# Kernel optimization log

Measured on AMD Instinct MI355X. Metric: run time of the kernel, lower is better.

## Reference

```python
import jax, jax.numpy as jnp
import numpy as np

B = 32
SIZES = [5023, 1256, 314, 79]
NS = [s + 1 for s in SIZES]   # padded vertex counts per level: [5024,1257,315,80]
K = 9
ENC_C = [3, 64, 128, 256]
DEC_C = [256, 128, 64, 3]
LATENT = 256


def _feast(x, nbr, wm, bm, wc, bc, act):
    # x: [B,N,F]; nbr: [N,K] int32 (col 0 = self index)
    xn = jnp.transpose(x[:, nbr, :], (0, 1, 3, 2))          # [B,N,F,K]
    xr = xn - xn[..., :1]                                    # relative to self neighbor
    logits = jnp.einsum('bnfk,of->bnok', xr, wm) + bm[None, None, :, None]  # conv1d(F->K,1)
    perm = jax.nn.softmax(logits, axis=2)                    # softmax over out-channel dim (torch dim=1)
    agg = jnp.einsum('bnfk,bnko->bnfo', xn, perm)            # [B,N,F,K] batched matmul
    Bv, N, F, Kv = agg.shape
    y = act(agg.reshape(Bv, N, F * Kv) @ wc.T + bc)          # linear(F*K -> out)
    mask = jnp.ones((N, 1), y.dtype).at[-1, 0].set(0.0)      # zero out padding vertex
    return y * mask


def _pool(x, L):
    # x: [B,M,F]; L: [Mp,M] -> [B,Mp,F]  (dense form of torch.spmm pooling)
    return jnp.einsum('pm,bmf->bpf', L, x)


def _forward(x, nbrs, Ds, Us, enc_p, dec_p, fce_w, fce_b, fcd_w, fcd_b):
    elu = jax.nn.elu
    ident = lambda v: v
    for i in range(3):
        wm, bm, wc, bc = enc_p[i]
        x = _feast(x, nbrs[i], wm, bm, wc, bc, elu)
        x = _pool(x, Ds[i])
    z = x.reshape(B, -1) @ fce_w.T + fce_b                    # [B, latent]
    x = (z @ fcd_w.T + fcd_b).reshape(B, NS[3], DEC_C[0])
    dec_nbrs = [nbrs[2], nbrs[1], nbrs[0]]
    dec_Us = [Us[2], Us[1], Us[0]]
    acts = [elu, elu, ident]                                  # last dconv uses identity
    for i in range(3):
        x = _pool(x, dec_Us[i])
        wm, bm, wc, bc = dec_p[i]
        x = _feast(x, dec_nbrs[i], wm, bm, wc, bc, acts[i])
    return x


def setup_inputs() -> dict:
    key = jax.random.key(0)
    ks = iter(jax.random.split(key, 64))
    nrm = lambda sh, s=0.05: jax.random.normal(next(ks), sh, dtype=jnp.float32) * s
    inp = {}
    inp['x'] = jax.random.normal(next(ks), (B, NS[0], 3), dtype=jnp.float32)
    for i in range(3):
        n = NS[i]
        nb = jax.random.randint(next(ks), (n, K), 0, n)
        nb = nb.at[:, 0].set(jnp.arange(n))
        inp[f'nbr{i}'] = nb.astype(jnp.int32)
    for i in range(3):
        cols = jax.random.randint(next(ks), (NS[i + 1],), 0, NS[i])
        inp[f'D{i}'] = jax.nn.one_hot(cols, NS[i], dtype=jnp.float32)   # sparse-like pooling
        cols_u = jax.random.randint(next(ks), (NS[i],), 0, NS[i + 1])
        inp[f'U{i}'] = jax.nn.one_hot(cols_u, NS[i + 1], dtype=jnp.float32)
    for i in range(3):
        fi, fo = ENC_C[i], ENC_C[i + 1]
        inp[f'e{i}_wm'] = nrm((K, fi)); inp[f'e{i}_bm'] = jnp.zeros((K,), jnp.float32)
        inp[f'e{i}_wc'] = nrm((fo, fi * K)); inp[f'e{i}_bc'] = jnp.zeros((fo,), jnp.float32)
    inp['fce_w'] = nrm((LATENT, NS[3] * ENC_C[3])); inp['fce_b'] = jnp.zeros((LATENT,), jnp.float32)
    inp['fcd_w'] = nrm((NS[3] * DEC_C[0], LATENT)); inp['fcd_b'] = jnp.zeros((NS[3] * DEC_C[0],), jnp.float32)
    for i in range(3):
        fi, fo = DEC_C[i], DEC_C[i + 1]
        inp[f'd{i}_wm'] = nrm((K, fi)); inp[f'd{i}_bm'] = jnp.zeros((K,), jnp.float32)
        inp[f'd{i}_wc'] = nrm((fo, fi * K)); inp[f'd{i}_bc'] = jnp.zeros((fo,), jnp.float32)
    return inp


def reference(x, nbr0, nbr1, nbr2, D0, D1, D2, U0, U1, U2,
              e0_wm, e0_bm, e0_wc, e0_bc, e1_wm, e1_bm, e1_wc, e1_bc,
              e2_wm, e2_bm, e2_wc, e2_bc, fce_w, fce_b, fcd_w, fcd_b,
              d0_wm, d0_bm, d0_wc, d0_bc, d1_wm, d1_bm, d1_wc, d1_bc,
              d2_wm, d2_bm, d2_wc, d2_bc):
    nbrs = [nbr0, nbr1, nbr2]
    Ds = [D0, D1, D2]
    Us = [U0, U1, U2]
    enc_p = [(e0_wm, e0_bm, e0_wc, e0_bc), (e1_wm, e1_bm, e1_wc, e1_bc), (e2_wm, e2_bm, e2_wc, e2_bc)]
    dec_p = [(d0_wm, d0_bm, d0_wc, d0_bc), (d1_wm, d1_bm, d1_wc, d1_bc), (d2_wm, d2_bm, d2_wc, d2_bc)]
    return _forward(x, nbrs, Ds, Us, enc_p, dec_p, fce_w, fce_b, fcd_w, fcd_b)
```

## Files before the change

### kernel.cpp

```cpp
#include <hip/hip_runtime.h>
#include <cstddef>

#define KN 9
typedef unsigned short u16;
typedef unsigned int u32;
typedef __attribute__((ext_vector_type(8))) short short8;
typedef __attribute__((ext_vector_type(4))) float f32x4;

__device__ inline u16 f2b(float f) {
    union { float f; u32 u; } v; v.f = f;
    u32 r = v.u + 0x7FFFu + ((v.u >> 16) & 1u);
    return (u16)(r >> 16);
}
__device__ inline float b2f(u16 h) {
    union { u32 u; float f; } v; v.u = ((u32)h) << 16; return v.f;
}

__device__ inline int xcd_swz(int bid, int n) {
    int q = n >> 3, r = n & 7;
    int x = bid & 7, pos = bid >> 3;
    return (x < r ? x * (q + 1) : r * (q + 1) + (x - r) * q) + pos;
}

__global__ void extract_idx_all(
    const float* __restrict__ D0, const float* __restrict__ D1, const float* __restrict__ D2,
    const float* __restrict__ U0, const float* __restrict__ U1, const float* __restrict__ U2,
    int* __restrict__ iD0, int* __restrict__ iD1, int* __restrict__ iD2,
    int* __restrict__ iU0, int* __restrict__ iU1, int* __restrict__ iU2)
{
    int blk = blockIdx.x;
    const float* L; int M; int* out; int p;
    if      (blk < 1257) { L = D0; M = 5024; out = iD0; p = blk; }
    else if (blk < 1572) { L = D1; M = 1257; out = iD1; p = blk - 1257; }
    else if (blk < 1652) { L = D2; M = 315;  out = iD2; p = blk - 1572; }
    else if (blk < 6676) { L = U0; M = 1257; out = iU0; p = blk - 1652; }
    else if (blk < 7933) { L = U1; M = 315;  out = iU1; p = blk - 6676; }
    else                 { L = U2; M = 80;   out = iU2; p = blk - 7933; }
    const float* row = L + (size_t)p * M;
    for (int m = threadIdx.x; m < M; m += 256)
        if (row[m] > 0.5f) out[p] = m;
}

__global__ void zero_f32(float4* __restrict__ p, int n4)
{
    int t = blockIdx.x * 256 + threadIdx.x;
    if (t < n4) p[t] = (float4){0.f, 0.f, 0.f, 0.f};
}

__device__ inline void wcr_one(const float* __restrict__ wc, u16* __restrict__ out, int t, int F) {
    int FK = F * KN;
    int c = t / FK, rem = t - c * FK, j = rem / F, f = rem - j * F;
    out[t] = f2b(wc[(size_t)c * FK + f * KN + j]);
}
__device__ inline void wg_one(const float* __restrict__ wc, u16* __restrict__ out, int t, int F, int C) {
    int n = t / F, f = t - n * F;
    int j = n / C, c = n - j * C;
    out[t] = f2b(wc[(size_t)c * (F * KN) + f * KN + j]);
}
__device__ inline void ccw_one(const float* __restrict__ wm, u16* __restrict__ out, int t, int F) {
    int n = t / F, f = t - n * F;
    out[t] = (n < KN) ? f2b(wm[n * F + f]) : (u16)0;
}
__global__ void cvt_weights(
    const float* __restrict__ e1_wc, const float* __restrict__ e2_wc,
    const float* __restrict__ d0_wc, const float* __restrict__ d1_wc,
    const float* __restrict__ e1_wm, const float* __restrict__ e2_wm,
    const float* __restrict__ d0_wm, const float* __restrict__ d1_wm,
    const float* __restrict__ d2_wm, const float* __restrict__ d2_wc,
    u16* __restrict__ wcrE1, u16* __restrict__ wcrE2,
    u16* __restrict__ wg0, u16* __restrict__ wg1,
    u16* __restrict__ ccwE1, u16* __restrict__ ccwE2,
    u16* __restrict__ ccwD0, u16* __restrict__ ccwD1,
    u16* __restrict__ w3, float* __restrict__ zbuf)
{
    int t = blockIdx.x * 256 + threadIdx.x;
    if (t < 73728)  { wcr_one(e1_wc, wcrE1, t, 64);       return; } t -= 73728;
    if (t < 294912) { wcr_one(e2_wc, wcrE2, t, 128);      return; } t -= 294912;
    if (t < 294912) { wg_one(d0_wc, wg0, t, 256, 128);    return; } t -= 294912;
    if (t < 73728)  { wg_one(d1_wc, wg1, t, 128, 64);     return; } t -= 73728;
    if (t < 4096)   { ccw_one(e1_wm, ccwE1, t, 64);       return; } t -= 4096;
    if (t < 8192)   { ccw_one(e2_wm, ccwE2, t, 128);      return; } t -= 8192;
    if (t < 16384)  { ccw_one(d0_wm, ccwD0, t, 256);      return; } t -= 16384;
    if (t < 8192)   { ccw_one(d1_wm, ccwD1, t, 128);      return; } t -= 8192;
    if (t < 4096) {
        int n = t >> 6, k = t & 63;
        float v = 0.f;
        if (n < KN) v = d2_wm[n * 64 + k];
        else if (n >= 9 && n < 36) {
            int cj = n - 9, j = cj / 3, c = cj - j * 3;
            v = d2_wc[(size_t)c * 576 + k * KN + j];
        }
        w3[t] = f2b(v);
        return;
    } t -= 4096;
    if (t < 8192) zbuf[t] = 0.f;
}

__global__ void compose_tables(
    const int* __restrict__ nbr0, const int* __restrict__ nbr1, const int* __restrict__ nbr2,
    const int* __restrict__ idxD1, const int* __restrict__ idxD2,
    const int* __restrict__ idxU0, const int* __restrict__ idxU1, const int* __restrict__ idxU2,
    int* __restrict__ nbrD1, int* __restrict__ nbrD2,
    int* __restrict__ nbrU2, int* __restrict__ nbrU1, int* __restrict__ nbrU0,
    int* __restrict__ maskE1, int* __restrict__ maskE2)
{
    int t = blockIdx.x * 256 + threadIdx.x;
    if (t < 2835)  { int p = t / 9, j = t - p * 9; nbrD1[p * 12 + j] = nbr1[idxD1[p] * 9 + j]; return; } t -= 2835;
    if (t < 720)   { int p = t / 9, j = t - p * 9; nbrD2[p * 12 + j] = nbr2[idxD2[p] * 9 + j]; return; } t -= 720;
    if (t < 2835)  { int p = t / 9, j = t - p * 9; nbrU2[p * 12 + j] = idxU2[nbr2[p * 9 + j]]; return; } t -= 2835;
    if (t < 11313) { int p = t / 9, j = t - p * 9; nbrU1[p * 12 + j] = idxU1[nbr1[p * 9 + j]]; return; } t -= 11313;
    if (t < 45216) { int p = t / 9, j = t - p * 9; nbrU0[p * 12 + j] = idxU0[nbr0[p * 9 + j]]; return; } t -= 45216;
    if (t < 315)   { maskE1[t] = (idxD1[t] == 1256) ? 1 : 0; return; } t -= 315;
    if (t < 80)    { maskE2[t] = (idxD2[t] == 314) ? 1 : 0; }
}

template<int NW, int OS>
__global__ __launch_bounds__(256) void cc_gemm(
    const u16* __restrict__ A, const u16* __restrict__ W,
    float* __restrict__ out, int M, int F)
{
    __shared__ u16 As[64 * 72];
    __shared__ u16 Ws[64 * 72];
    int tid = threadIdx.x;
    int mT = blockIdx.x * 64;
    int wid = tid >> 6, lane = tid & 63;
    int wr = wid >> 1, wcq = wid & 1;
    int r = lane & 15, g = lane >> 4;
    f32x4 acc[2][2];
    #pragma unroll
    for (int i = 0; i < 2; ++i)
        #pragma unroll
        for (int j = 0; j < 2; ++j)
            acc[i][j] = (f32x4){0.f, 0.f, 0.f, 0.f};

    for (int k0 = 0; k0 < F; k0 += 64) {
        #pragma unroll
// ... 49 lines not shown
    int wr = wid >> 1, wcq = wid & 1;
    int r = lane & 15, g = lane >> 4;
    f32x4 acc[2][2];
    #pragma unroll
    for (int i = 0; i < 2; ++i)
        #pragma unroll
        for (int j = 0; j < 2; ++j)
            acc[i][j] = (f32x4){0.f, 0.f, 0.f, 0.f};

    {
        #pragma unroll
        for (int h = 0; h < 2; ++h) {
            int gi = tid + h * 256;
            int m = gi >> 3, kg = gi & 7;
            uint4 va = {0u, 0u, 0u, 0u};
            int row = mT + m;
            if (row < M) va = *(const uint4*)(A + (size_t)row * 64 + kg * 8);
            *(uint4*)&As[m * 72 + kg * 8] = va;
            *(uint4*)&Ws[m * 72 + kg * 8] = *(const uint4*)(W + (size_t)m * 64 + kg * 8);
        }
        __syncthreads();
        #pragma unroll
        for (int S = 0; S < 2; ++S) {
            short8 af[2], bf[2];
            #pragma unroll
            for (int R = 0; R < 2; ++R)
                af[R] = *(const short8*)&As[(wr * 32 + R * 16 + r) * 72 + S * 32 + g * 8];
            #pragma unroll
            for (int C2 = 0; C2 < 2; ++C2)
                bf[C2] = *(const short8*)&Ws[(wcq * 32 + C2 * 16 + r) * 72 + S * 32 + g * 8];
            #pragma unroll
            for (int R = 0; R < 2; ++R)
                #pragma unroll
                for (int C2 = 0; C2 < 2; ++C2)
                    acc[R][C2] = __builtin_amdgcn_mfma_f32_16x16x32_bf16(af[R], bf[C2], acc[R][C2], 0, 0, 0);
        }
    }
    #pragma unroll
    for (int R = 0; R < 2; ++R)
        #pragma unroll
        for (int C2 = 0; C2 < 2; ++C2)
            #pragma unroll
            for (int q = 0; q < 4; ++q) {
                int mm = mT + wr * 32 + R * 16 + g * 4 + q;
                if (mm >= M) continue;
                int nn = wcq * 32 + C2 * 16 + r;
                if (nn >= 36) continue;
                int b = mm / 1257, p = mm - b * 1257;
                float val = acc[R][C2][q];
                if (nn < 9) {
                    CCT[((size_t)p * 9 + nn) * 32 + b] = val;
                } else {
                    int cj = nn - 9, j = cj / 3, c = cj - j * 3;
                    GWT[(size_t)p * 864 + j * 96 + b * 3 + c] = val;
                }
            }
}

template<int ACT, int MASK>
__global__ __launch_bounds__(256) void lin_gemm(
    const u16* __restrict__ A, const u16* __restrict__ W,
    const float* __restrict__ bias, u16* __restrict__ Y,
    const int* __restrict__ maskT,
    int M, int K, int N, int P)
{
    __shared__ u16 As[2][64 * 72];
    __shared__ u16 Ws[2][64 * 72];
    int tid = threadIdx.x;
    int mT = blockIdx.x * 64, nT = blockIdx.y * 64;
    int wid = tid >> 6, lane = tid & 63;
    int wr = wid >> 1, wcq = wid & 1;
    int r = lane & 15, g = lane >> 4;
    int lm = tid >> 3, lkg = tid & 7;
    f32x4 acc[2][2];
    #pragma unroll
    for (int i = 0; i < 2; ++i)
        #pragma unroll
        for (int j = 0; j < 2; ++j)
            acc[i][j] = (f32x4){0.f, 0.f, 0.f, 0.f};

    uint4 ra[2], rw[2];
    #pragma unroll
    for (int h = 0; h < 2; ++h) {
        int m = lm + h * 32;
        int row = mT + m;
        uint4 z; z.x = z.y = z.z = z.w = 0u;
        ra[h] = (row < M) ? *(const uint4*)(A + (size_t)row * K + lkg * 8) : z;
        rw[h] = *(const uint4*)(W + (size_t)(nT + m) * K + lkg * 8);
    }
    #pragma unroll
    for (int h = 0; h < 2; ++h) {
        int m = lm + h * 32;
        *(uint4*)&As[0][m * 72 + lkg * 8] = ra[h];
        *(uint4*)&Ws[0][m * 72 + lkg * 8] = rw[h];
    }

    int cur = 0;
    for (int k0 = 0; k0 < K; k0 += 64) {
        __syncthreads();
        bool more = (k0 + 64 < K);
        if (more) {
            int kn = k0 + 64;
            #pragma unroll
            for (int h = 0; h < 2; ++h) {
                int m = lm + h * 32;
                int row = mT + m;
                uint4 z; z.x = z.y = z.z = z.w = 0u;
// ... 56 lines not shown
    int wid = tid >> 6, lane = tid & 63;
    int wr = wid >> 1, wcq = wid & 1;
    int r = lane & 15, g = lane >> 4;
    f32x4 acc[2][2];
    #pragma unroll
    for (int i = 0; i < 2; ++i)
        #pragma unroll
        for (int j = 0; j < 2; ++j)
            acc[i][j] = (f32x4){0.f, 0.f, 0.f, 0.f};

    for (int s = 0; s < KSTEPS; ++s) {
        int k0 = kbase + s * 64;
        #pragma unroll
        for (int h = 0; h < 2; ++h) {
            int gi = tid + h * 256;
            int m = gi >> 3, kg = gi & 7;
            uint4 va = {0u, 0u, 0u, 0u};
            int row = mT + m;
            if (row < M) va = *(const uint4*)(A + (size_t)row * K + k0 + kg * 8);
            *(uint4*)&As[m * 72 + kg * 8] = va;
            *(uint4*)&Ws[m * 72 + kg * 8] = *(const uint4*)(W + (size_t)(nT + m) * K + k0 + kg * 8);
        }
        __syncthreads();
        #pragma unroll
        for (int S = 0; S < 2; ++S) {
            short8 af[2], bf[2];
            #pragma unroll
            for (int R = 0; R < 2; ++R)
                af[R] = *(const short8*)&As[(wr * 32 + R * 16 + r) * 72 + S * 32 + g * 8];
            #pragma unroll
            for (int C2 = 0; C2 < 2; ++C2)
                bf[C2] = *(const short8*)&Ws[(wcq * 32 + C2 * 16 + r) * 72 + S * 32 + g * 8];
            #pragma unroll
            for (int R = 0; R < 2; ++R)
                #pragma unroll
                for (int C2 = 0; C2 < 2; ++C2)
                    acc[R][C2] = __builtin_amdgcn_mfma_f32_16x16x32_bf16(af[R], bf[C2], acc[R][C2], 0, 0, 0);
        }
        __syncthreads();
    }
    #pragma unroll
    for (int R = 0; R < 2; ++R)
        #pragma unroll
        for (int C2 = 0; C2 < 2; ++C2)
            #pragma unroll
            for (int q = 0; q < 4; ++q) {
                int mm = mT + wr * 32 + R * 16 + g * 4 + q;
                if (mm >= M) continue;
                int nn = nT + wcq * 32 + C2 * 16 + r;
                atomicAdd(&Yf[(size_t)mm * N + nn], acc[R][C2][q]);
            }
}

__global__ __launch_bounds__(256) void elu_mask_cvt(
    const float* __restrict__ Yf, const float* __restrict__ bias,
    const int* __restrict__ maskT, u16* __restrict__ Y,
    int M, int N, int P)
{
    int t = blockIdx.x * 256 + threadIdx.x;
    int tot = (M * N) >> 2;
    if (t >= tot) return;
    int e0 = t * 4;
    int m = e0 / N, n0 = e0 - m * N;
    float4 v = ((const float4*)Yf)[t];
    float o0 = v.x + bias[n0];
    float o1 = v.y + bias[n0 + 1];
    float o2 = v.z + bias[n0 + 2];
    float o3 = v.w + bias[n0 + 3];
    o0 = o0 > 0.f ? o0 : expm1f(o0);
    o1 = o1 > 0.f ? o1 : expm1f(o1);
    o2 = o2 > 0.f ? o2 : expm1f(o2);
    o3 = o3 > 0.f ? o3 : expm1f(o3);
    if (maskT[m % P] != 0) { o0 = 0.f; o1 = 0.f; o2 = 0.f; o3 = 0.f; }
    uint2 o;
    o.x = (u32)f2b(o0) | ((u32)f2b(o1) << 16);
    o.y = (u32)f2b(o2) | ((u32)f2b(o3) << 16);
    ((uint2*)Y)[t] = o;
}

__global__ __launch_bounds__(256) void fce_mfma(
    const u16* __restrict__ A, const float* __restrict__ Wf,
    const float* __restrict__ bias, float* __restrict__ z)
{
    __shared__ u16 As[32 * 72];
    __shared__ u16 Ws[64 * 72];
    int tid = threadIdx.x;
    int nT = blockIdx.x * 64;
    int kbase = blockIdx.y * 256;
    int wv = tid >> 6, lane = tid & 63;
    int r = lane & 15, g = lane >> 4;
    int m = tid >> 3, kg = tid & 7;
    f32x4 acc[2];
    acc[0] = (f32x4){0.f, 0.f, 0.f, 0.f};
    acc[1] = (f32x4){0.f, 0.f, 0.f, 0.f};

    for (int ks = 0; ks < 4; ++ks) {
        int k0 = kbase + ks * 64;
        *(uint4*)&As[m * 72 + kg * 8] = *(const uint4*)(A + (size_t)m * 20480 + k0 + kg * 8);
        #pragma unroll
        for (int h = 0; h < 2; ++h) {
            int row = m + h * 32;
            const float* wr2 = Wf + (size_t)(nT + row) * 20480 + k0 + kg * 8;
            float4 w0 = *(const float4*)(wr2);
            float4 w1 = *(const float4*)(wr2 + 4);
            u16 o[8] = { f2b(w0.x), f2b(w0.y), f2b(w0.z), f2b(w0.w),
                         f2b(w1.x), f2b(w1.y), f2b(w1.z), f2b(w1.w) };
            *(uint4*)&Ws[row * 72 + kg * 8] = *(const uint4*)o;
        }
        __syncthreads();
        #pragma unroll
        for (int S = 0; S < 2; ++S) {
            short8 bfr = *(const short8*)&Ws[(wv * 16 + r) * 72 + S * 32 + g * 8];
            #pragma unroll
            for (int R = 0; R < 2; ++R) {
                short8 af = *(const short8*)&As[(R * 16 + r) * 72 + S * 32 + g * 8];
                acc[R] = __builtin_amdgcn_mfma_f32_16x16x32_bf16(af, bfr, acc[R], 0, 0, 0);
            }
        }
        __syncthreads();
    }
    #pragma unroll
    for (int R = 0; R < 2; ++R)
        #pragma unroll
        for (int q = 0; q < 4; ++q) {
            int mm = R * 16 + g * 4 + q;
            int nn = nT + wv * 16 + r;
            float v = acc[R][q];
            if (blockIdx.y == 0) v += bias[nn];
            atomicAdd(&z[mm * 256 + nn], v);
        }
// ... 88 lines not shown
    if (aw && lane < KN) s_nb[wid][lane] = b * Pin + nbrT[p * 12 + lane];
    __syncthreads();

    if (aw && lane < KN) {
        int j = lane;
        const float* c0 = cc + (size_t)s_nb[wid][0] * 16;
        const float* cj = cc + (size_t)s_nb[wid][j] * 16;
        float L[KN];
        #pragma unroll
        for (int i = 0; i < KN; ++i) L[i] = bm[i] + cj[i] - c0[i];
        float mx = L[0];
        #pragma unroll
        for (int i = 1; i < KN; ++i) mx = fmaxf(mx, L[i]);
        float s = 0.f;
        #pragma unroll
        for (int i = 0; i < KN; ++i) { L[i] = __expf(L[i] - mx); s += L[i]; }
        float inv = 1.f / s;
        #pragma unroll
        for (int i = 0; i < KN; ++i) s_p[wid][i * KN + j] = L[i] * inv;
    }
    __syncthreads();

    if (aw) {
        float xn[KN][FC];
        #pragma unroll
        for (int i = 0; i < KN; ++i) {
            const u16* xr = x + (size_t)s_nb[wid][i] * F;
            #pragma unroll
            for (int c = 0; c < FC; ++c) xn[i][c] = b2f(xr[lane + c * 64]);
        }
        #pragma unroll
        for (int j = 0; j < KN; ++j) {
            float a[FC];
            #pragma unroll
            for (int c = 0; c < FC; ++c) a[c] = 0.f;
            #pragma unroll
            for (int i = 0; i < KN; ++i) {
                float pv = s_p[wid][i * KN + j];
                #pragma unroll
                for (int c = 0; c < FC; ++c) a[c] += xn[i][c] * pv;
            }
            u16* orow = agg + (size_t)row * (KN * F) + j * F;
            #pragma unroll
            for (int c = 0; c < FC; ++c) orow[lane + c * 64] = f2b(a[c]);
        }
    }
}

template<int C>
__global__ __launch_bounds__(256, 4) void mix_feast_v(
    const u16* __restrict__ G, const float* __restrict__ cc,
    const int* __restrict__ nbrT, const float* __restrict__ bm,
    const float* __restrict__ bc, u16* __restrict__ y,
    int Pin, int P, int Mtot)
{
    constexpr int LPR = C / 8;
    constexpr int RPW = 64 / LPR;
    constexpr int RPB = 4 * RPW;
    constexpr int GS = KN * C;
    __shared__ float s_p[RPB][84];
    __shared__ int   s_nb[RPB][KN];

    int tid = threadIdx.x, wid = tid >> 6, lane = tid & 63;
    int rowbase = xcd_swz(blockIdx.x, gridDim.x) * RPB;

    for (int t = tid; t < RPB * KN; t += 256) {
        int rr = t / KN, j = t - rr * KN;
        int row = rowbase + rr;
        int v = 0;
        if (row < Mtot) {
            int b = row / P, p = row - b * P;
            v = b * Pin + nbrT[p * 12 + j];
        }
        s_nb[rr][j] = v;
    }
    __syncthreads();

    {
        int rl, j0;
        if (C == 64) { rl = wid * RPW + (lane >> 3); j0 = lane & 7; }
        else         { rl = wid * RPW + (lane >> 4); j0 = lane & 15; }
        int row = rowbase + rl;
        if (row < Mtot && j0 <= KN) {
            float cc0[KN], bmr[KN];
            const float* c0 = cc + (size_t)s_nb[rl][0] * 16;
            #pragma unroll
            for (int i = 0; i < KN; ++i) { cc0[i] = c0[i]; bmr[i] = bm[i]; }
            int nj = 1;
            int jl[2]; jl[0] = j0; jl[1] = -1;
            if (C == 64 && j0 == 0) { jl[1] = 8; nj = 2; }
            if (j0 >= KN) nj = 0;
            for (int t = 0; t < nj; ++t) {
                int j = jl[t];
                const float* cj = cc + (size_t)s_nb[rl][j] * 16;
                float L[KN];
                #pragma unroll
                for (int i = 0; i < KN; ++i) L[i] = bmr[i] + cj[i] - cc0[i];
                float mx = L[0];
                #pragma unroll
                for (int i = 1; i < KN; ++i) mx = fmaxf(mx, L[i]);
                float sm = 0.f;
                #pragma unroll
                for (int i = 0; i < KN; ++i) { L[i] = __expf(L[i] - mx); sm += L[i]; }
                float inv = 1.f / sm;
                #pragma unroll
                for (int i = 0; i < KN; ++i) s_p[rl][i * KN + j] = L[i] * inv;
            }
        }
    }
    __syncthreads();

    {
        int rl = wid * RPW + lane / LPR;
        int coff = (lane % LPR) * 8;
        int row = rowbase + rl;
        if (row >= Mtot) return;
        int b = row / P, p = row - b * P;
        (void)b;
        float acc[8];
        #pragma unroll
        for (int k = 0; k < 8; ++k) acc[k] = bc[coff + k];
        #pragma unroll 1
        for (int i = 0; i < KN; ++i) {
            const u16* gr = G + (size_t)s_nb[rl][i] * GS + coff;
            #pragma unroll
            for (int j = 0; j < KN; ++j) {
                uint4 gv = *(const uint4*)(gr + j * C);
                const u16* ge = (const u16*)&gv;
                float p0 = s_p[rl][i * KN + j];
                #pragma unroll
                for (int k = 0; k < 8; ++k) acc[k] += p0 * b2f(ge[k]);
            }
        }
        u16 o[8];
        #pragma unroll
        for (int k = 0; k < 8; ++k) {
            float v = acc[k];
            v = v > 0.f ? v : expm1f(v);
            if (p == P - 1) v = 0.f;
            o[k] = f2b(v);
        }
        *(uint4*)(y + (size_t)row * C + coff) = *(const uint4*)o;
    }
}

__global__ __launch_bounds__(256) void feast_e0(
    const float* __restrict__ x, const int* __restrict__ nbr,
    const int* __restrict__ sel,
    const float* __restrict__ wm, const float* __restrict__ bm,
    const float* __restrict__ wcw, const float* __restrict__ bc,
    u16* __restrict__ y,
    int Nin, int P, int Nlevel, int Mtot)
{
    constexpr int F = 3, C = 64, FS = 4, Q = 27;
    __shared__ float s_wm[KN * FS];
    __shared__ float s_wc[C * Q];
    __shared__ float s_bm[KN];
    __shared__ float s_xn[4][KN * FS];
    __shared__ float s_lg[4][81];
    __shared__ float s_pm[4][81];
    __shared__ float s_ag[4][Q];
    __shared__ int   s_idx[4][KN];

    int tid = threadIdx.x, wid = tid >> 6, lane = tid & 63;
    for (int t = tid; t < KN * F; t += 256) { int i = t / F, f = t - i * F; s_wm[i * FS + f] = wm[t]; }
    for (int t = tid; t < C * Q; t += 256) s_wc[t] = wcw[t];
    if (tid < KN) s_bm[tid] = bm[tid];

    int wg = xcd_swz(blockIdx.x, gridDim.x) * 4 + wid;
    bool aw = wg < Mtot;
    int b = 0, p = 0, n = 0;
    if (aw) {
        b = wg / P; p = wg - b * P;
        n = sel[p];
    }
    if (aw && lane < KN) s_idx[wid][lane] = nbr[n * KN + lane];
    __syncthreads();

    if (aw) {
        const float* xb = x + (size_t)b * Nin * F;
        for (int t = lane; t < KN * F; t += 64) {
            int i = t / F, f = t - i * F;
            s_xn[wid][i * FS + f] = xb[(size_t)s_idx[wid][i] * F + f];
        }
    }
    __syncthreads();

    if (aw) {
        for (int pr = lane; pr < 81; pr += 64) {
            int i = pr / KN, j = pr - i * KN;
            float acc = s_bm[i];
            for (int f = 0; f < F; ++f)
                acc += (s_xn[wid][j * FS + f] - s_xn[wid][f]) * s_wm[i * FS + f];
            s_lg[wid][pr] = acc;
        }
    }
    __syncthreads();

    if (aw && lane < KN) {
        int j = lane;
        float mx = -1e30f;
        #pragma unroll
        for (int i = 0; i < KN; ++i) mx = fmaxf(mx, s_lg[wid][i * KN + j]);
        float sm = 0.f, ev[KN];
        #pragma unroll
        for (int i = 0; i < KN; ++i) { ev[i] = __expf(s_lg[wid][i * KN + j] - mx); sm += ev[i]; }
        float inv = 1.f / sm;
        #pragma unroll
        for (int i = 0; i < KN; ++i) s_pm[wid][i * KN + j] = ev[i] * inv;
    }
    __syncthreads();

    if (aw) {
        for (int t = lane; t < Q; t += 64) {
            int f = t / KN, j = t - f * KN;
            float acc = 0.f;
            #pragma unroll
            for (int i = 0; i < KN; ++i) acc += s_xn[wid][i * FS + f] * s_pm[wid][i * KN + j];
            s_ag[wid][t] = acc;
        }
    }
    __syncthreads();

    if (aw) {
        int c = lane;
        float acc = 0.f;
        #pragma unroll
        for (int q = 0; q < Q; ++q)
            acc += s_wc[c * Q + q] * s_ag[wid][q];
        float val = acc + bc[c];
        val = val > 0.f ? val : expm1f(val);
        if (n == Nlevel - 1) val = 0.f;
        y[(size_t)wg * C + c] = f2b(val);
    }
}

__global__ __launch_bounds__(256) void mix_d2t(
    const float* __restrict__ CCT, const float* __restrict__ GWT,
    const int* __restrict__ nbrT,
    const float* __restrict__ bm9, const float* __restrict__ bc3,
    float* __restrict__ out)
{
    __shared__ float s_out[8][32][3];
    int tid = threadIdx.x, wid = tid >> 6, lane = tid & 63;
    int sub = lane >> 5, b = lane & 31;
    int vbase = xcd_swz(blockIdx.x, gridDim.x) * 8;
    int v = vbase + wid * 2 + sub;

    int nbi[KN];
    #pragma unroll
    for (int i = 0; i < KN; ++i) nbi[i] = nbrT[v * 12 + i];
    float bmr[KN];
    #pragma unroll
    for (int i = 0; i < KN; ++i) bmr[i] = bm9[i];

    float cc0[KN];
    {
        const float* c0 = CCT + (size_t)nbi[0] * 9 * 32 + b;
        #pragma unroll
        for (int f = 0; f < KN; ++f) cc0[f] = c0[f * 32];
    }
    float a0 = bc3[0], a1 = bc3[1], a2 = bc3[2];
    #pragma unroll
    for (int j = 0; j < KN; ++j) {
        const float* cj = CCT + (size_t)nbi[j] * 9 * 32 + b;
        float L[KN];
        #pragma unroll
        for (int i = 0; i < KN; ++i) L[i] = bmr[i] + cj[i * 32] - cc0[i];
        float mx = L[0];
        #pragma unroll
        for (int i = 1; i < KN; ++i) mx = fmaxf(mx, L[i]);
        float sm = 0.f;
        #pragma unroll
        for (int i = 0; i < KN; ++i) { L[i] = __expf(L[i] - mx); sm += L[i]; }
        float inv = 1.f / sm;
        #pragma unroll
        for (int i = 0; i < KN; ++i) {
            float pv = L[i] * inv;
            const float* g = GWT + (size_t)nbi[i] * 864 + j * 96 + b * 3;
            a0 += pv * g[0];
            a1 += pv * g[1];
            a2 += pv * g[2];
        }
    }
    if (v == 5023) { a0 = 0.f; a1 = 0.f; a2 = 0.f; }
    s_out[wid * 2 + sub][b][0] = a0;
    s_out[wid * 2 + sub][b][1] = a1;
    s_out[wid * 2 + sub][b][2] = a2;
    __syncthreads();
    {
        int bb = tid >> 3, vi = tid & 7;
        float* dst = out + ((size_t)bb * 5024 + vbase + vi) * 3;
        dst[0] = s_out[vi][bb][0];
        dst[1] = s_out[vi][bb][1];
        dst[2] = s_out[vi][bb][2];
    }
}

extern "C" void kernel_launch(void* const* d_in, const int* in_sizes, int n_in,
                              void* d_out, int out_size, void* d_ws, size_t ws_size,
                              hipStream_t stream)
{
    const float* x     = (const float*)d_in[0];
    const int*   nbr0  = (const int*)d_in[1];
    const int*   nbr1  = (const int*)d_in[2];
    const int*   nbr2  = (const int*)d_in[3];
    const float* D0    = (const float*)d_in[4];
    const float* U0    = (const float*)d_in[5];
    const float* D1    = (const float*)d_in[6];
    const float* U1    = (const float*)d_in[7];
    const float* D2    = (const float*)d_in[8];
    const float* U2    = (const float*)d_in[9];
    const float* e0_wm = (const float*)d_in[10]; const float* e0_bm = (const float*)d_in[11];
    const float* e0_wc = (const float*)d_in[12]; const float* e0_bc = (const float*)d_in[13];
    const float* e1_wm = (const float*)d_in[14]; const float* e1_bm = (const float*)d_in[15];
    const float* e1_wc = (const float*)d_in[16]; const float* e1_bc = (const float*)d_in[17];
    const float* e2_wm = (const float*)d_in[18]; const float* e2_bm = (const float*)d_in[19];
    const float* e2_wc = (const float*)d_in[20]; const float* e2_bc = (const float*)d_in[21];
    const float* fce_w = (const float*)d_in[22]; const float* fce_b = (const float*)d_in[23];
    const float* fcd_w = (const float*)d_in[24]; const float* fcd_b = (const float*)d_in[25];
    const float* d0_wm = (const float*)d_in[26]; const float* d0_bm = (const float*)d_in[27];
    const float* d0_wc = (const float*)d_in[28]; const float* d0_bc = (const float*)d_in[29];
    const float* d1_wm = (const float*)d_in[30]; const float* d1_bm = (const float*)d_in[31];
    const float* d1_wc = (const float*)d_in[32]; const float* d1_bc = (const float*)d_in[33];
    const float* d2_wm = (const float*)d_in[34]; const float* d2_bm = (const float*)d_in[35];
    const float* d2_wc = (const float*)d_in[36]; const float* d2_bc = (const float*)d_in[37];

    char* w = (char*)d_ws;
    int* idxD0 = (int*)(w);
    int* idxD1 = idxD0 + 1257;
    int* idxD2 = idxD1 + 315;
    int* idxU0 = idxD2 + 80;
    int* idxU1 = idxU0 + 5024;
    int* idxU2 = idxU1 + 1257;
    int* nbrD1  = (int*)(w + 33024);
    int* nbrD2  = (int*)(w + 48144);
    int* nbrU2  = (int*)(w + 51984);
    int* nbrU1  = (int*)(w + 67104);
    int* nbrU0  = (int*)(w + 127440);
    int* maskE1 = (int*)(w + 368640);
    int* maskE2 = (int*)(w + 369920);
    u16* wcrE1 = (u16*)(w + 370432);
    u16* wcrE2 = (u16*)(w + 517888);
    u16* wg0   = (u16*)(w + 1107712);
    u16* wg1   = (u16*)(w + 1697536);
    u16* ccwE1 = (u16*)(w + 1844992);
    u16* ccwE2 = (u16*)(w + 1853184);
    u16* ccwD0 = (u16*)(w + 1869568);
    u16* ccwD1 = (u16*)(w + 1902336);
    u16* w3    = (u16*)(w + 1918720);
    float* zbuf = (float*)(w + 1926912);

    u16*   X1   = (u16*)  (w + 2097152);
    float* CC1  = (float*)(w + 7245824);
    u16*   AGG1 = (u16*)  (w + 9820160);
    u16*   X2   = (u16*)  (w + 21432320);
    float* CC2  = (float*)(w + 24012800);
    u16*   AGG2 = (u16*)  (w + 24657920);
    u16*   X3   = (u16*)  (w + 2097152);
    u16*   X3P  = (u16*)  (w + 3407872);
    float* CCD0 = (float*)(w + 4718592);
    u16*   G0   = (u16*)  (w + 4882432);
    u16*   XD1P = (u16*)  (w + 10780672);
    float* CCD1 = (float*)(w + 13361152);
    u16*   G1   = (u16*)  (w + 14006272);
    u16*   XD2P = (u16*)  (w + 25618432);
    float* CCT  = (float*)(w + 30767104);
    float* GWT  = (float*)(w + 32215168);
    float* X2F  = (float*)(w + 36559360);
    float* X3F  = (float*)(w + 41720320);

    extract_idx_all<<<8248, 256, 0, stream>>>(D0, D1, D2, U0, U1, U2,
                                              idxD0, idxD1, idxD2, idxU0, idxU1, idxU2);
    cvt_weights<<<3072, 256, 0, stream>>>(e1_wc, e2_wc, d0_wc, d1_wc,
                                          e1_wm, e2_wm, d0_wm, d1_wm, d2_wm, d2_wc,
                                          wcrE1, wcrE2, wg0, wg1,
                                          ccwE1, ccwE2, ccwD0, ccwD1, w3, zbuf);
    compose_tables<<<248, 256, 0, stream>>>(nbr0, nbr1, nbr2,
                                            idxD1, idxD2, idxU0, idxU1, idxU2,
                                            nbrD1, nbrD2, nbrU2, nbrU1, nbrU0,
                                            maskE1, maskE2);
    zero_f32<<<1900, 256, 0, stream>>>((float4*)X2F, 486400);

    feast_e0<<<10056, 256, 0, stream>>>(x, nbr0, idxD0, e0_wm, e0_bm, e0_wc, e0_bc,
                                        X1, 5024, 1257, 5024, 40224);
    cc_gemm<16, 16><<<629, 256, 0, stream>>>(X1, ccwE1, CC1, 40224, 64);
    feast_agg<64><<<2520, 256, 0, stream>>>(X1, CC1, nbrD1, e1_bm, AGG1, 1257, 315, 10080);
    lin_gemm_sk<<<dim3(158, 2, 3), 256, 0, stream>>>(AGG1, wcrE1, X2F, 10080, 576, 128, 3);
    elu_mask_cvt<<<1260, 256, 0, stream>>>(X2F, e1_bc, maskE1, X2, 10080, 128, 315);
    cc_gemm<16, 16><<<158, 256, 0, stream>>>(X2, ccwE2, CC2, 10080, 128);
    feast_agg<128><<<640, 256, 0, stream>>>(X2, CC2, nbrD2, e2_bm, AGG2, 315, 80, 2560);
    lin_gemm_sk<<<dim3(40, 4, 6), 256, 0, stream>>>(AGG2, wcrE2, X3F, 2560, 1152, 256, 3);
    elu_mask_cvt<<<640, 256, 0, stream>>>(X3F, e2_bc, maskE2, X3, 2560, 256, 80);

    fce_mfma<<<dim3(4, 80), 256, 0, stream>>>(X3, fce_w, fce_b, zbuf);
    fcd_mfma<<<320, 256, 0, stream>>>(zbuf, fcd_w, fcd_b, X3P);

    cc_gemm<16, 16><<<40, 256, 0, stream>>>(X3P, ccwD0, CCD0, 2560, 256);
    lin_gemm<0, 0><<<dim3(40, 18), 256, 0, stream>>>(X3P, wg0, nullptr, G0, nullptr,
                                                     2560, 256, 1152, 1);
    mix_feast_v<128><<<630, 256, 0, stream>>>(G0, CCD0, nbrU2, d0_bm, d0_bc, XD1P,
                                              80, 315, 10080);
    cc_gemm<16, 16><<<158, 256, 0, stream>>>(XD1P, ccwD1, CCD1, 10080, 128);
    lin_gemm<0, 0><<<dim3(158, 9), 256, 0, stream>>>(XD1P, wg1, nullptr, G1, nullptr,
                                                     10080, 128, 576, 1);
    mix_feast_v<64><<<1257, 256, 0, stream>>>(G1, CCD1, nbrU1, d1_bm, d1_bc, XD2P,
                                              315, 1257, 40224);
    cc_gemmT<<<629, 256, 0, stream>>>(XD2P, w3, CCT, GWT, 40224);
    mix_d2t<<<628, 256, 0, stream>>>(CCT, GWT, nbrU0, d2_bm, d2_bc, (float*)d_out);
}
```

Measured before the change: 236.2 us.

## Fuse per-vertex softmax-logit projections into producer epilogues, pad GWT to float4

Removes three separate cc_gemm launches by computing the 9 logit projections (x·wm) inside the epilogues of feast_e0, elu_mask_cvt and mix_feast_v<128>, using warp shuffle reductions over fp32 values. It also drops the corresponding bf16 weight conversions, and pads the GWT layout from stride 3 to stride 4 so mix_d2t can use float4 loads. The aim is to cut kernel launches and re-reads of the activations. The cost is extra shuffle work and shared-memory loads in the producers. The projections now use fp32 activations rather than bf16-rounded ones, which slightly changes numerics.

```diff
diff --git a/kernel.cpp b/kernel.cpp
--- a/kernel.cpp
+++ b/kernel.cpp
@@ -64,24 +64,18 @@
 __global__ void cvt_weights(
     const float* __restrict__ e1_wc, const float* __restrict__ e2_wc,
     const float* __restrict__ d0_wc, const float* __restrict__ d1_wc,
-    const float* __restrict__ e1_wm, const float* __restrict__ e2_wm,
-    const float* __restrict__ d0_wm, const float* __restrict__ d1_wm,
-    const float* __restrict__ d2_wm, const float* __restrict__ d2_wc,
+    const float* __restrict__ d0_wm, const float* __restrict__ d2_wm,
+    const float* __restrict__ d2_wc,
     u16* __restrict__ wcrE1, u16* __restrict__ wcrE2,
     u16* __restrict__ wg0, u16* __restrict__ wg1,
-    u16* __restrict__ ccwE1, u16* __restrict__ ccwE2,
-    u16* __restrict__ ccwD0, u16* __restrict__ ccwD1,
-    u16* __restrict__ w3, float* __restrict__ zbuf)
+    u16* __restrict__ ccwD0, u16* __restrict__ w3, float* __restrict__ zbuf)
 {
     int t = blockIdx.x * 256 + threadIdx.x;
     if (t < 73728)  { wcr_one(e1_wc, wcrE1, t, 64);       return; } t -= 73728;
     if (t < 294912) { wcr_one(e2_wc, wcrE2, t, 128);      return; } t -= 294912;
     if (t < 294912) { wg_one(d0_wc, wg0, t, 256, 128);    return; } t -= 294912;
     if (t < 73728)  { wg_one(d1_wc, wg1, t, 128, 64);     return; } t -= 73728;
-    if (t < 4096)   { ccw_one(e1_wm, ccwE1, t, 64);       return; } t -= 4096;
-    if (t < 8192)   { ccw_one(e2_wm, ccwE2, t, 128);      return; } t -= 8192;
     if (t < 16384)  { ccw_one(d0_wm, ccwD0, t, 256);      return; } t -= 16384;
-    if (t < 8192)   { ccw_one(d1_wm, ccwD1, t, 128);      return; } t -= 8192;
     if (t < 4096) {
         int n = t >> 6, k = t & 63;
         float v = 0.f;
@@ -237,7 +231,7 @@
                     CCT[((size_t)p * 9 + nn) * 32 + b] = val;
                 } else {
                     int cj = nn - 9, j = cj / 3, c = cj - j * 3;
-                    GWT[(size_t)p * 864 + j * 96 + b * 3 + c] = val;
+                    GWT[(size_t)p * 1152 + j * 128 + b * 4 + c] = val;
                 }
             }
 }
@@ -400,30 +394,53 @@
             }
 }
 
+template<int WITHCC>
 __global__ __launch_bounds__(256) void elu_mask_cvt(
     const float* __restrict__ Yf, const float* __restrict__ bias,
     const int* __restrict__ maskT, u16* __restrict__ Y,
+    const float* __restrict__ wmcc, float* __restrict__ ccout,
     int M, int N, int P)
 {
     int t = blockIdx.x * 256 + threadIdx.x;
     int tot = (M * N) >> 2;
-    if (t >= tot) return;
-    int e0 = t * 4;
+    bool act = t < tot;
+    int e0 = act ? t * 4 : 0;
     int m = e0 / N, n0 = e0 - m * N;
-    float4 v = ((const float4*)Yf)[t];
-    float o0 = v.x + bias[n0];
-    float o1 = v.y + bias[n0 + 1];
-    float o2 = v.z + bias[n0 + 2];
-    float o3 = v.w + bias[n0 + 3];
-    o0 = o0 > 0.f ? o0 : expm1f(o0);
-    o1 = o1 > 0.f ? o1 : expm1f(o1);
-    o2 = o2 > 0.f ? o2 : expm1f(o2);
-    o3 = o3 > 0.f ? o3 : expm1f(o3);
-    if (maskT[m % P] != 0) { o0 = 0.f; o1 = 0.f; o2 = 0.f; o3 = 0.f; }
-    uint2 o;
-    o.x = (u32)f2b(o0) | ((u32)f2b(o1) << 16);
-    o.y = (u32)f2b(o2) | ((u32)f2b(o3) << 16);
-    ((uint2*)Y)[t] = o;
+    float o0 = 0.f, o1 = 0.f, o2 = 0.f, o3 = 0.f;
+    if (act) {
+        float4 v = ((const float4*)Yf)[t];
+        o0 = v.x + bias[n0];
+        o1 = v.y + bias[n0 + 1];
+        o2 = v.z + bias[n0 + 2];
+        o3 = v.w + bias[n0 + 3];
+        o0 = o0 > 0.f ? o0 : expm1f(o0);
+        o1 = o1 > 0.f ? o1 : expm1f(o1);
+        o2 = o2 > 0.f ? o2 : expm1f(o2);
+        o3 = o3 > 0.f ? o3 : expm1f(o3);
+        if (maskT[m % P] != 0) { o0 = 0.f; o1 = 0.f; o2 = 0.f; o3 = 0.f; }
+        uint2 o;
+        o.x = (u32)f2b(o0) | ((u32)f2b(o1) << 16);
+        o.y = (u32)f2b(o2) | ((u32)f2b(o3) << 16);
+        ((uint2*)Y)[t] = o;
+    }
+    if (WITHCC) {
+        int lane = threadIdx.x & 63;
+        #pragma unroll
+        for (int i = 0; i < KN; ++i) {
+            float pr = 0.f;
+            if (act) {
+                const float* wr2 = wmcc + i * 128 + n0;
+                pr = o0 * wr2[0] + o1 * wr2[1] + o2 * wr2[2] + o3 * wr2[3];
+            }
+            pr += __shfl_xor(pr, 16, 64);
+            pr += __shfl_xor(pr, 8, 64);
+            pr += __shfl_xor(pr, 4, 64);
+            pr += __shfl_xor(pr, 2, 64);
+            pr += __shfl_xor(pr, 1, 64);
+            if (act && (lane & 31) == 0)
+                ccout[(size_t)m * 16 + i] = pr;
+        }
+    }
 }
 
 __global__ __launch_bounds__(256) void fce_mfma(
@@ -618,6 +635,7 @@
     const u16* __restrict__ G, const float* __restrict__ cc,
     const int* __restrict__ nbrT, const float* __restrict__ bm,
     const float* __restrict__ bc, u16* __restrict__ y,
+    const float* __restrict__ wmcc, float* __restrict__ ccout,
     int Pin, int P, int Mtot)
 {
     constexpr int LPR = C / 8;
@@ -626,10 +644,14 @@
     constexpr int GS = KN * C;
     __shared__ float s_p[RPB][84];
     __shared__ int   s_nb[RPB][KN];
+    __shared__ float s_wm[KN * 128];
 
     int tid = threadIdx.x, wid = tid >> 6, lane = tid & 63;
     int rowbase = xcd_swz(blockIdx.x, gridDim.x) * RPB;
 
+    if (ccout) {
+        for (int t = tid; t < KN * C; t += 256) s_wm[t] = wmcc[t];
+    }
     for (int t = tid; t < RPB * KN; t += 256) {
         int rr = t / KN, j = t - rr * KN;
         int row = rowbase + rr;
@@ -698,15 +720,32 @@
                 for (int k = 0; k < 8; ++k) acc[k] += p0 * b2f(ge[k]);
             }
         }
+        float vp[8];
         u16 o[8];
         #pragma unroll
         for (int k = 0; k < 8; ++k) {
             float v = acc[k];
             v = v > 0.f ? v : expm1f(v);
             if (p == P - 1) v = 0.f;
+            vp[k] = v;
             o[k] = f2b(v);
         }
         *(uint4*)(y + (size_t)row * C + coff) = *(const uint4*)o;
+        if (C == 128 && ccout) {
+            #pragma unroll
+            for (int i = 0; i < KN; ++i) {
+                const float* wr2 = s_wm + i * 128 + coff;
+                float pr = 0.f;
+                #pragma unroll
+                for (int k = 0; k < 8; ++k) pr += vp[k] * wr2[k];
+                pr += __shfl_xor(pr, 8, 64);
+                pr += __shfl_xor(pr, 4, 64);
+                pr += __shfl_xor(pr, 2, 64);
+                pr += __shfl_xor(pr, 1, 64);
+                if ((lane & 15) == 0)
+                    ccout[(size_t)row * 16 + i] = pr;
+            }
+        }
     }
 }
 
@@ -715,6 +754,7 @@
     const int* __restrict__ sel,
     const float* __restrict__ wm, const float* __restrict__ bm,
     const float* __restrict__ wcw, const float* __restrict__ bc,
+    const float* __restrict__ wm1, float* __restrict__ cc1,
     u16* __restrict__ y,
     int Nin, int P, int Nlevel, int Mtot)
 {
@@ -722,6 +762,7 @@
     __shared__ float s_wm[KN * FS];
     __shared__ float s_wc[C * Q];
     __shared__ float s_bm[KN];
+    __shared__ float s_wm1[KN * 64];
     __shared__ float s_xn[4][KN * FS];
     __shared__ float s_lg[4][81];
     __shared__ float s_pm[4][81];
@@ -731,6 +772,7 @@
     int tid = threadIdx.x, wid = tid >> 6, lane = tid & 63;
     for (int t = tid; t < KN * F; t += 256) { int i = t / F, f = t - i * F; s_wm[i * FS + f] = wm[t]; }
     for (int t = tid; t < C * Q; t += 256) s_wc[t] = wcw[t];
+    for (int t = tid; t < KN * 64; t += 256) s_wm1[t] = wm1[t];
     if (tid < KN) s_bm[tid] = bm[tid];
 
     int wg = xcd_swz(blockIdx.x, gridDim.x) * 4 + wid;
@@ -798,6 +840,17 @@
         val = val > 0.f ? val : expm1f(val);
         if (n == Nlevel - 1) val = 0.f;
         y[(size_t)wg * C + c] = f2b(val);
+        #pragma unroll
+        for (int i = 0; i < KN; ++i) {
+            float pr = val * s_wm1[i * 64 + lane];
+            pr += __shfl_xor(pr, 32, 64);
+            pr += __shfl_xor(pr, 16, 64);
+            pr += __shfl_xor(pr, 8, 64);
+            pr += __shfl_xor(pr, 4, 64);
+            pr += __shfl_xor(pr, 2, 64);
+            pr += __shfl_xor(pr, 1, 64);
+            if (lane == 0) cc1[(size_t)wg * 16 + i] = pr;
+        }
     }
 }
 
@@ -843,10 +896,10 @@
         #pragma unroll
         for (int i = 0; i < KN; ++i) {
             float pv = L[i] * inv;
-            const float* g = GWT + (size_t)nbi[i] * 864 + j * 96 + b * 3;
-            a0 += pv * g[0];
-            a1 += pv * g[1];
-            a2 += pv * g[2];
+            float4 g = *(const float4*)(GWT + (size_t)nbi[i] * 1152 + j * 128 + b * 4);
+            a0 += pv * g.x;
+            a1 += pv * g.y;
+            a2 += pv * g.z;
         }
     }
     if (v == 5023) { a0 = 0.f; a1 = 0.f; a2 = 0.f; }
@@ -910,12 +963,9 @@
     u16* wcrE2 = (u16*)(w + 517888);
     u16* wg0   = (u16*)(w + 1107712);
     u16* wg1   = (u16*)(w + 1697536);
-    u16* ccwE1 = (u16*)(w + 1844992);
-    u16* ccwE2 = (u16*)(w + 1853184);
-    u16* ccwD0 = (u16*)(w + 1869568);
-    u16* ccwD1 = (u16*)(w + 1902336);
-    u16* w3    = (u16*)(w + 1918720);
-    float* zbuf = (float*)(w + 1926912);
+    u16* ccwD0 = (u16*)(w + 1844992);
+    u16* w3    = (u16*)(w + 1877760);
+    float* zbuf = (float*)(w + 1886208);
 
     u16*   X1   = (u16*)  (w + 2097152);
     float* CC1  = (float*)(w + 7245824);
@@ -933,15 +983,14 @@
     u16*   XD2P = (u16*)  (w + 25618432);
     float* CCT  = (float*)(w + 30767104);
     float* GWT  = (float*)(w + 32215168);
-    float* X2F  = (float*)(w + 36559360);
-    float* X3F  = (float*)(w + 41720320);
+    float* X2F  = (float*)(w + 38007424);
+    float* X3F  = (float*)(w + 43168384);
 
     extract_idx_all<<<8248, 256, 0, stream>>>(D0, D1, D2, U0, U1, U2,
                                               idxD0, idxD1, idxD2, idxU0, idxU1, idxU2);
     cvt_weights<<<3072, 256, 0, stream>>>(e1_wc, e2_wc, d0_wc, d1_wc,
-                                          e1_wm, e2_wm, d0_wm, d1_wm, d2_wm, d2_wc,
-                                          wcrE1, wcrE2, wg0, wg1,
-                                          ccwE1, ccwE2, ccwD0, ccwD1, w3, zbuf);
+                                          d0_wm, d2_wm, d2_wc,
+                                          wcrE1, wcrE2, wg0, wg1, ccwD0, w3, zbuf);
     compose_tables<<<248, 256, 0, stream>>>(nbr0, nbr1, nbr2,
                                             idxD1, idxD2, idxU0, idxU1, idxU2,
                                             nbrD1, nbrD2, nbrU2, nbrU1, nbrU0,
@@ -949,15 +998,15 @@
     zero_f32<<<1900, 256, 0, stream>>>((float4*)X2F, 486400);
 
     feast_e0<<<10056, 256, 0, stream>>>(x, nbr0, idxD0, e0_wm, e0_bm, e0_wc, e0_bc,
-                                        X1, 5024, 1257, 5024, 40224);
-    cc_gemm<16, 16><<<629, 256, 0, stream>>>(X1, ccwE1, CC1, 40224, 64);
+                                        e1_wm, CC1, X1, 5024, 1257, 5024, 40224);
     feast_agg<64><<<2520, 256, 0, stream>>>(X1, CC1, nbrD1, e1_bm, AGG1, 1257, 315, 10080);
     lin_gemm_sk<<<dim3(158, 2, 3), 256, 0, stream>>>(AGG1, wcrE1, X2F, 10080, 576, 128, 3);
-    elu_mask_cvt<<<1260, 256, 0, stream>>>(X2F, e1_bc, maskE1, X2, 10080, 128, 315);
-    cc_gemm<16, 16><<<158, 256, 0, stream>>>(X2, ccwE2, CC2, 10080, 128);
+    elu_mask_cvt<1><<<1260, 256, 0, stream>>>(X2F, e1_bc, maskE1, X2, e2_wm, CC2,
+                                              10080, 128, 315);
     feast_agg<128><<<640, 256, 0, stream>>>(X2, CC2, nbrD2, e2_bm, AGG2, 315, 80, 2560);
     lin_gemm_sk<<<dim3(40, 4, 6), 256, 0, stream>>>(AGG2, wcrE2, X3F, 2560, 1152, 256, 3);
-    elu_mask_cvt<<<640, 256, 0, stream>>>(X3F, e2_bc, maskE2, X3, 2560, 256, 80);
+    elu_mask_cvt<0><<<640, 256, 0, stream>>>(X3F, e2_bc, maskE2, X3, nullptr, nullptr,
+                                             2560, 256, 80);
 
     fce_mfma<<<dim3(4, 80), 256, 0, stream>>>(X3, fce_w, fce_b, zbuf);
     fcd_mfma<<<320, 256, 0, stream>>>(zbuf, fcd_w, fcd_b, X3P);
@@ -966,12 +1015,11 @@
     lin_gemm<0, 0><<<dim3(40, 18), 256, 0, stream>>>(X3P, wg0, nullptr, G0, nullptr,
                                                      2560, 256, 1152, 1);
     mix_feast_v<128><<<630, 256, 0, stream>>>(G0, CCD0, nbrU2, d0_bm, d0_bc, XD1P,
-                                              80, 315, 10080);
-    cc_gemm<16, 16><<<158, 256, 0, stream>>>(XD1P, ccwD1, CCD1, 10080, 128);
+                                              d1_wm, CCD1, 80, 315, 10080);
     lin_gemm<0, 0><<<dim3(158, 9), 256, 0, stream>>>(XD1P, wg1, nullptr, G1, nullptr,
                                                      10080, 128, 576, 1);
     mix_feast_v<64><<<1257, 256, 0, stream>>>(G1, CCD1, nbrU1, d1_bm, d1_bc, XD2P,
-                                              315, 1257, 40224);
+                                              nullptr, nullptr, 315, 1257, 40224);
     cc_gemmT<<<629, 256, 0, stream>>>(XD2P, w3, CCT, GWT, 40224);
     mix_d2t<<<628, 256, 0, stream>>>(CCT, GWT, nbrU0, d2_bm, d2_bc, (float*)d_out);
 }
```

Result: slower. 256.3 us (+8.5%).

## Transpose input to vertex-major and batch all 32 samples per block in first FeaSt

Applied to the files above, without the earlier changes.

Adds a transpose kernel that lays out x as [vertex][batch][feature], so one block can gather the 9 neighbours for a pooled vertex across all 32 batch entries in contiguous reads. The first encoder FeaSt now uses one block per selected vertex (1257 blocks) instead of one wave per (batch, vertex), and loads the 64x27 weight matrix into shared memory once per block rather than once per 4 rows. Each thread computes 8 output channels and writes them with a 16-byte store. The cost is an extra transpose launch and buffer, and only one of every eight threads does the softmax and aggregation stage.

```diff
diff --git a/kernel.cpp b/kernel.cpp
--- a/kernel.cpp
+++ b/kernel.cpp
@@ -45,6 +45,15 @@
 {
     int t = blockIdx.x * 256 + threadIdx.x;
     if (t < n4) p[t] = (float4){0.f, 0.f, 0.f, 0.f};
+}
+
+__global__ void xpose_x(const float* __restrict__ x, float* __restrict__ xt)
+{
+    int t = blockIdx.x * 256 + threadIdx.x;
+    if (t >= 482304) return;
+    int f = t % 3; int rem = t / 3;
+    int n = rem % 5024; int b = rem / 5024;
+    xt[((size_t)n * 32 + b) * 3 + f] = x[t];
 }
 
 __device__ inline void wcr_one(const float* __restrict__ wc, u16* __restrict__ out, int t, int F) {
@@ -710,94 +719,85 @@
     }
 }
 
-__global__ __launch_bounds__(256) void feast_e0(
-    const float* __restrict__ x, const int* __restrict__ nbr,
+__global__ __launch_bounds__(256) void feast_e0p(
+    const float* __restrict__ xt, const int* __restrict__ nbr,
     const int* __restrict__ sel,
     const float* __restrict__ wm, const float* __restrict__ bm,
-    const float* __restrict__ wcw, const float* __restrict__ bc,
-    u16* __restrict__ y,
-    int Nin, int P, int Nlevel, int Mtot)
-{
-    constexpr int F = 3, C = 64, FS = 4, Q = 27;
-    __shared__ float s_wm[KN * FS];
-    __shared__ float s_wc[C * Q];
+    const float* __restrict__ wc, const float* __restrict__ bc,
+    u16* __restrict__ y)
+{
+    __shared__ float s_x[KN][96];
+    __shared__ float s_wc[64 * 27];
+    __shared__ float s_agg[27][33];
+    __shared__ float s_wm[27];
     __shared__ float s_bm[KN];
-    __shared__ float s_xn[4][KN * FS];
-    __shared__ float s_lg[4][81];
-    __shared__ float s_pm[4][81];
-    __shared__ float s_ag[4][Q];
-    __shared__ int   s_idx[4][KN];
-
-    int tid = threadIdx.x, wid = tid >> 6, lane = tid & 63;
-    for (int t = tid; t < KN * F; t += 256) { int i = t / F, f = t - i * F; s_wm[i * FS + f] = wm[t]; }
-    for (int t = tid; t < C * Q; t += 256) s_wc[t] = wcw[t];
+    __shared__ int   s_nb[KN];
+
+    int tid = threadIdx.x;
+    int p = xcd_swz(blockIdx.x, gridDim.x);
+    int n = sel[p];
+    for (int t = tid; t < 64 * 27; t += 256) s_wc[t] = wc[t];
+    if (tid < 27) s_wm[tid] = wm[tid];
     if (tid < KN) s_bm[tid] = bm[tid];
-
-    int wg = xcd_swz(blockIdx.x, gridDim.x) * 4 + wid;
-    bool aw = wg < Mtot;
-    int b = 0, p = 0, n = 0;
-    if (aw) {
-        b = wg / P; p = wg - b * P;
-        n = sel[p];
-    }
-    if (aw && lane < KN) s_idx[wid][lane] = nbr[n * KN + lane];
+    if (tid < KN) s_nb[tid] = nbr[n * KN + tid];
     __syncthreads();
-
-    if (aw) {
-        const float* xb = x + (size_t)b * Nin * F;
-        for (int t = lane; t < KN * F; t += 64) {
-            int i = t / F, f = t - i * F;
-            s_xn[wid][i * FS + f] = xb[(size_t)s_idx[wid][i] * F + f];
-        }
+    for (int t = tid; t < KN * 96; t += 256) {
+        int i = t / 96, rr = t - i * 96;
+        s_x[i][rr] = xt[(size_t)s_nb[i] * 96 + rr];
     }
     __syncthreads();
 
-    if (aw) {
-        for (int pr = lane; pr < 81; pr += 64) {
-            int i = pr / KN, j = pr - i * KN;
-            float acc = s_bm[i];
-            for (int f = 0; f < F; ++f)
-                acc += (s_xn[wid][j * FS + f] - s_xn[wid][f]) * s_wm[i * FS + f];
-            s_lg[wid][pr] = acc;
+    int b = tid >> 3, cg = tid & 7;
+    if (cg == 0) {
+        float x00 = s_x[0][b * 3], x01 = s_x[0][b * 3 + 1], x02 = s_x[0][b * 3 + 2];
+        #pragma unroll 1
+        for (int j = 0; j < KN; ++j) {
+            float d0 = s_x[j][b * 3]     - x00;
+            float d1 = s_x[j][b * 3 + 1] - x01;
+            float d2 = s_x[j][b * 3 + 2] - x02;
+            float L[KN];
+            #pragma unroll
+            for (int i = 0; i < KN; ++i)
+                L[i] = s_bm[i] + d0 * s_wm[i * 3] + d1 * s_wm[i * 3 + 1] + d2 * s_wm[i * 3 + 2];
+            float mx = L[0];
+            #pragma unroll
+            for (int i = 1; i < KN; ++i) mx = fmaxf(mx, L[i]);
+            float sm = 0.f;
+            #pragma unroll
+            for (int i = 0; i < KN; ++i) { L[i] = __expf(L[i] - mx); sm += L[i]; }
+            float inv = 1.f / sm;
+            #pragma unroll
+            for (int f = 0; f < 3; ++f) {
+                float a = 0.f;
+                #pragma unroll
+                for (int i = 0; i < KN; ++i) a += (L[i] * inv) * s_x[i][b * 3 + f];
+                s_agg[f * KN + j][b] = a;
+            }
         }
     }
     __syncthreads();
 
-    if (aw && lane < KN) {
-        int j = lane;
-        float mx = -1e30f;
-        #pragma unroll
-        for (int i = 0; i < KN; ++i) mx = fmaxf(mx, s_lg[wid][i * KN + j]);
-        float sm = 0.f, ev[KN];
-        #pragma unroll
-        for (int i = 0; i < KN; ++i) { ev[i] = __expf(s_lg[wid][i * KN + j] - mx); sm += ev[i]; }
-        float inv = 1.f / sm;
-        #pragma unroll
-        for (int i = 0; i < KN; ++i) s_pm[wid][i * KN + j] = ev[i] * inv;
-    }
-    __syncthreads();
-
-    if (aw) {
-        for (int t = lane; t < Q; t += 64) {
-            int f = t / KN, j = t - f * KN;
-            float acc = 0.f;
-            #pragma unroll
-            for (int i = 0; i < KN; ++i) acc += s_xn[wid][i * FS + f] * s_pm[wid][i * KN + j];
-            s_ag[wid][t] = acc;
-        }
-    }
-    __syncthreads();
-
-    if (aw) {
-        int c = lane;
-        float acc = 0.f;
-        #pragma unroll
-        for (int q = 0; q < Q; ++q)
-            acc += s_wc[c * Q + q] * s_ag[wid][q];
-        float val = acc + bc[c];
-        val = val > 0.f ? val : expm1f(val);
-        if (n == Nlevel - 1) val = 0.f;
-        y[(size_t)wg * C + c] = f2b(val);
+    {
+        int c0 = cg * 8;
+        float acc[8];
+        #pragma unroll
+        for (int k = 0; k < 8; ++k) acc[k] = 0.f;
+        #pragma unroll 1
+        for (int q = 0; q < 27; ++q) {
+            float a = s_agg[q][b];
+            #pragma unroll
+            for (int k = 0; k < 8; ++k) acc[k] += s_wc[(c0 + k) * 27 + q] * a;
+        }
+        u16 o[8];
+        #pragma unroll
+        for (int k = 0; k < 8; ++k) {
+            float v = acc[k] + bc[c0 + k];
+            v = v > 0.f ? v : expm1f(v);
+            if (n == 5023) v = 0.f;
+            o[k] = f2b(v);
+        }
+        size_t row = (size_t)b * 1257 + p;
+        *(uint4*)(y + row * 64 + c0) = *(const uint4*)o;
     }
 }
 
@@ -935,6 +935,7 @@
     float* GWT  = (float*)(w + 32215168);
     float* X2F  = (float*)(w + 36559360);
     float* X3F  = (float*)(w + 41720320);
+    float* XT   = (float*)(w + 44341760);
 
     extract_idx_all<<<8248, 256, 0, stream>>>(D0, D1, D2, U0, U1, U2,
                                               idxD0, idxD1, idxD2, idxU0, idxU1, idxU2);
@@ -947,9 +948,9 @@
                                             nbrD1, nbrD2, nbrU2, nbrU1, nbrU0,
                                             maskE1, maskE2);
     zero_f32<<<1900, 256, 0, stream>>>((float4*)X2F, 486400);
-
-    feast_e0<<<10056, 256, 0, stream>>>(x, nbr0, idxD0, e0_wm, e0_bm, e0_wc, e0_bc,
-                                        X1, 5024, 1257, 5024, 40224);
+    xpose_x<<<1884, 256, 0, stream>>>(x, XT);
+
+    feast_e0p<<<1257, 256, 0, stream>>>(XT, nbr0, idxD0, e0_wm, e0_bm, e0_wc, e0_bc, X1);
     cc_gemm<16, 16><<<629, 256, 0, stream>>>(X1, ccwE1, CC1, 40224, 64);
     feast_agg<64><<<2520, 256, 0, stream>>>(X1, CC1, nbrD1, e1_bm, AGG1, 1257, 315, 10080);
     lin_gemm_sk<<<dim3(158, 2, 3), 256, 0, stream>>>(AGG1, wcrE1, X2F, 10080, 576, 128, 3);
```

Measured after the change: 232.6 us. About the same (-1.5%).
